# Kernel tuning notes

Hardware: AMD Instinct MI355X
Metric: run time of the kernel (lower is better)

Reference implementation:

```python
import jax, jax.numpy as jnp
import numpy as np

D_MODEL = 1024
NUM_HEADS = 16
HEAD_DIM = D_MODEL // NUM_HEADS
D_FF = 4096
LN_EPS = 1e-6  # flax nnx.LayerNorm default


def setup_inputs() -> dict:
    key = jax.random.key(0)
    ks = jax.random.split(key, 13)
    s_in = 1.0 / np.sqrt(D_MODEL)
    s_ff = 1.0 / np.sqrt(D_FF)
    return {
        "x": jax.random.normal(ks[0], (2, 2048, D_MODEL), dtype=jnp.float32),
        "Wq": jax.random.normal(ks[1], (D_MODEL, D_MODEL), jnp.float32) * s_in,
        "bq": jnp.zeros((D_MODEL,), jnp.float32),
        "Wk": jax.random.normal(ks[2], (D_MODEL, D_MODEL), jnp.float32) * s_in,
        "bk": jnp.zeros((D_MODEL,), jnp.float32),
        "Wv": jax.random.normal(ks[3], (D_MODEL, D_MODEL), jnp.float32) * s_in,
        "bv": jnp.zeros((D_MODEL,), jnp.float32),
        "Wo": jax.random.normal(ks[4], (D_MODEL, D_MODEL), jnp.float32) * s_in,
        "bo": jnp.zeros((D_MODEL,), jnp.float32),
        "W1": jax.random.normal(ks[5], (D_MODEL, D_FF), jnp.float32) * s_in,
        "b1": jnp.zeros((D_FF,), jnp.float32),
        "W2": jax.random.normal(ks[6], (D_FF, D_MODEL), jnp.float32) * s_ff,
        "b2": jnp.zeros((D_MODEL,), jnp.float32),
        "ln1_scale": jnp.ones((D_MODEL,), jnp.float32),
        "ln1_bias": jnp.zeros((D_MODEL,), jnp.float32),
        "ln2_scale": jnp.ones((D_MODEL,), jnp.float32),
        "ln2_bias": jnp.zeros((D_MODEL,), jnp.float32),
    }


def layer_norm(x, scale, bias):
    mu = jnp.mean(x, axis=-1, keepdims=True)
    var = jnp.mean(jnp.square(x - mu), axis=-1, keepdims=True)
    return (x - mu) * jax.lax.rsqrt(var + LN_EPS) * scale + bias


def reference(x, Wq, bq, Wk, bk, Wv, bv, Wo, bo, W1, b1, W2, b2,
              ln1_scale, ln1_bias, ln2_scale, ln2_bias):
    B, S, _ = x.shape
    h = layer_norm(x, ln1_scale, ln1_bias)
    # project and split heads: [B, H, S, Dh]
    q = (h @ Wq + bq).reshape(B, S, NUM_HEADS, HEAD_DIM).transpose(0, 2, 1, 3)
    k = (h @ Wk + bk).reshape(B, S, NUM_HEADS, HEAD_DIM).transpose(0, 2, 1, 3)
    v = (h @ Wv + bv).reshape(B, S, NUM_HEADS, HEAD_DIM).transpose(0, 2, 1, 3)
    scores = jnp.einsum("bhqd,bhkd->bhqk", q, k) / jnp.sqrt(jnp.float32(HEAD_DIM))
    attn = jax.nn.softmax(scores, axis=-1)
    out = jnp.einsum("bhqk,bhkd->bhqd", attn, v)
    out = out.transpose(0, 2, 1, 3).reshape(B, S, D_MODEL)
    x = x + out @ Wo + bo
    h2 = layer_norm(x, ln2_scale, ln2_bias)
    ff = jax.nn.relu(h2 @ W1 + b1) @ W2 + b2
    return x + ff
```

## Files before the change

kernel.cpp:

```cpp
#include <hip/hip_runtime.h>

typedef unsigned short ushort_t;
typedef __attribute__((ext_vector_type(8))) __bf16 bf16x8;
typedef __attribute__((ext_vector_type(8))) unsigned short ushort8v;
typedef __attribute__((ext_vector_type(4))) float floatx4;

__device__ inline float b2f(ushort_t u) {
    union { unsigned int i; float f; } c; c.i = ((unsigned int)u) << 16; return c.f;
}
__device__ inline ushort_t f2b(float f) {
    union { float f; unsigned int i; } c; c.f = f;
    unsigned int i = c.i;
    unsigned int r = (i + 0x7FFFu + ((i >> 16) & 1u)) >> 16;
    return (ushort_t)r;
}
__device__ inline bf16x8 as_bf16x8(ushort8v u) { return __builtin_bit_cast(bf16x8, u); }

__global__ __launch_bounds__(256) void concat3_kernel(
    const float* __restrict__ a, const float* __restrict__ b,
    const float* __restrict__ c, float* __restrict__ o) {
    int t = blockIdx.x * 256 + threadIdx.x;
    if (t < 3072)
        o[t] = t < 1024 ? a[t] : (t < 2048 ? b[t - 1024] : c[t - 2048]);
}

__global__ __launch_bounds__(256) void copy_f32_kernel(
    const float* __restrict__ src, float* __restrict__ dst) {
    size_t i = ((size_t)blockIdx.x * 256 + threadIdx.x) * 4;
    *(float4*)(dst + i) = *(const float4*)(src + i);
}

__global__ __launch_bounds__(256) void transpose_conv_kernel(
    const float* __restrict__ in, ushort_t* __restrict__ out,
    int R, int Csub, int ldin) {
    __shared__ float tile[32][33];
    int tx = threadIdx.x, ty = threadIdx.y;
    int r0 = blockIdx.y * 32, c0 = blockIdx.x * 32;
#pragma unroll
    for (int i = 0; i < 32; i += 8)
        tile[ty + i][tx] = in[(size_t)(r0 + ty + i) * ldin + c0 + tx];
    __syncthreads();
#pragma unroll
    for (int i = 0; i < 32; i += 8)
        out[(size_t)(c0 + ty + i) * R + r0 + tx] = f2b(tile[tx][ty + i]);
}

__global__ __launch_bounds__(256) void transpose_v_kernel(
    const ushort_t* __restrict__ qkv, ushort_t* __restrict__ vt) {
    __shared__ ushort_t tile[32][33];
    int tx = threadIdx.x, ty = threadIdx.y;
    int s0 = blockIdx.x * 32, d0 = blockIdx.y * 32;
    int bh = blockIdx.z, b = bh >> 4, h = bh & 15;
    const ushort_t* src = qkv + (size_t)b * 2048 * 3072 + 2048 + h * 64;
    ushort_t* dst = vt + (size_t)bh * 64 * 2048;
#pragma unroll
    for (int i = 0; i < 32; i += 8)
        tile[ty + i][tx] = src[(size_t)(s0 + ty + i) * 3072 + d0 + tx];
    __syncthreads();
#pragma unroll
    for (int i = 0; i < 32; i += 8)
        dst[(size_t)(d0 + ty + i) * 2048 + s0 + tx] = tile[tx][ty + i];
}

__device__ inline float wave_sum(float s) {
#pragma unroll
    for (int o = 32; o > 0; o >>= 1) s += __shfl_xor(s, o);
    return s;
}

__global__ __launch_bounds__(256) void ln_f32_kernel(
    const float* __restrict__ x, const float* __restrict__ sc,
    const float* __restrict__ bi, ushort_t* __restrict__ out) {
    int row = blockIdx.x, t = threadIdx.x;
    const float* xr = x + (size_t)row * 1024;
    float4 u = *(const float4*)(xr + t * 4);
    float v0 = u.x, v1 = u.y, v2 = u.z, v3 = u.w;
    __shared__ float sm[8];
    int wv = t >> 6, lane = t & 63;
    float s = wave_sum(v0 + v1 + v2 + v3);
    if (lane == 0) sm[wv] = s;
    __syncthreads();
    float mean = (sm[0] + sm[1] + sm[2] + sm[3]) * (1.0f / 1024.0f);
    float d0 = v0 - mean, d1 = v1 - mean, d2 = v2 - mean, d3 = v3 - mean;
    float q = wave_sum(d0 * d0 + d1 * d1 + d2 * d2 + d3 * d3);
    if (lane == 0) sm[4 + wv] = q;
    __syncthreads();
    float var = (sm[4] + sm[5] + sm[6] + sm[7]) * (1.0f / 1024.0f);
    float rn = rsqrtf(var + 1e-6f);
    float4 us = *(const float4*)(sc + t * 4);
    float4 ub = *(const float4*)(bi + t * 4);
    ushort4 o;
    o.x = f2b(d0 * rn * us.x + ub.x);
    o.y = f2b(d1 * rn * us.y + ub.y);
    o.z = f2b(d2 * rn * us.z + ub.z);
    o.w = f2b(d3 * rn * us.w + ub.w);
    *(ushort4*)(out + (size_t)row * 1024 + t * 4) = o;
}

__global__ __launch_bounds__(256) void gemm_bt_kernel(
    const ushort_t* __restrict__ A, const ushort_t* __restrict__ Bt,
    const float* __restrict__ bias, const float* __restrict__ resf,
    ushort_t* __restrict__ Cb, float* __restrict__ Cf,
    int M, int N, int K, int ldb, int op) {
    __shared__ __align__(16) ushort_t As[128 * 40];
    __shared__ __align__(16) ushort_t Bs[128 * 40];
    int tid = threadIdx.x;
    int m0 = blockIdx.y * 128, n0 = blockIdx.x * 128;
    int wv = tid >> 6, lane = tid & 63;
    int wr = wv & 1, wc = wv >> 1;
    int mo = wr * 64, no = wc * 64;
    int quad = lane >> 4, l16 = lane & 15;
    int k8 = quad * 8;

    floatx4 acc[4][4] = {};

    for (int k0 = 0; k0 < K; k0 += 32) {
#pragma unroll
        for (int c = 0; c < 2; ++c) {
            int e = c * 2048 + tid * 8;
            int r = e >> 5, kk = e & 31;
            *(ushort8v*)(As + r * 40 + kk) = *(const ushort8v*)(A + (size_t)(m0 + r) * K + k0 + kk);
            *(ushort8v*)(Bs + r * 40 + kk) = *(const ushort8v*)(Bt + (size_t)(n0 + r) * ldb + k0 + kk);
        }
        __syncthreads();
        bf16x8 af[4], bfr[4];
#pragma unroll
        for (int i = 0; i < 4; ++i) {
            af[i]  = as_bf16x8(*(const ushort8v*)(As + (mo + i * 16 + l16) * 40 + k8));
            bfr[i] = as_bf16x8(*(const ushort8v*)(Bs + (no + i * 16 + l16) * 40 + k8));
        }
#pragma unroll
        for (int mi = 0; mi < 4; ++mi)
#pragma unroll
            for (int ni = 0; ni < 4; ++ni)
                acc[mi][ni] = __builtin_amdgcn_mfma_f32_16x16x32_bf16(
                    af[mi], bfr[ni], acc[mi][ni], 0, 0, 0);
        __syncthreads();
    }

#pragma unroll
    for (int mi = 0; mi < 4; ++mi) {
#pragma unroll
        for (int r = 0; r < 4; ++r) {
            int row = m0 + mo + mi * 16 + quad * 4 + r;
            size_t rowoff = (size_t)row * N;
#pragma unroll
            for (int ni = 0; ni < 4; ++ni) {
                int col = n0 + no + ni * 16 + l16;
                float val = acc[mi][ni][r];
                if (op != 3) val += bias[col];
                if (op == 1) val = fmaxf(val, 0.0f);
                if (op >= 2) {
                    val += resf[rowoff + col];
                    Cf[rowoff + col] = val;
                } else {
                    Cb[rowoff + col] = f2b(val);
                }
            }
        }
    }
}

__global__ __launch_bounds__(256) void gemm_bt_atomic_kernel(
    const ushort_t* __restrict__ A, const ushort_t* __restrict__ Bt,
    const float* __restrict__ bias, float* __restrict__ Cf,
    int M, int N, int lda, int ldb, int Kc) {
    __shared__ __align__(16) ushort_t As[128 * 40];
    __shared__ __align__(16) ushort_t Bs[128 * 40];
    int tid = threadIdx.x;
    int m0 = blockIdx.y * 128, n0 = blockIdx.x * 128;
    int kbase = blockIdx.z * Kc;
    int wv = tid >> 6, lane = tid & 63;
    int wr = wv & 1, wc = wv >> 1;
    int mo = wr * 64, no = wc * 64;
    int quad = lane >> 4, l16 = lane & 15;
    int k8 = quad * 8;

    floatx4 acc[4][4] = {};

    for (int k0 = kbase; k0 < kbase + Kc; k0 += 32) {
#pragma unroll
        for (int c = 0; c < 2; ++c) {
            int e = c * 2048 + tid * 8;
            int r = e >> 5, kk = e & 31;
            *(ushort8v*)(As + r * 40 + kk) = *(const ushort8v*)(A + (size_t)(m0 + r) * lda + k0 + kk);
            *(ushort8v*)(Bs + r * 40 + kk) = *(const ushort8v*)(Bt + (size_t)(n0 + r) * ldb + k0 + kk);
        }
        __syncthreads();
        bf16x8 af[4], bfr[4];
#pragma unroll
        for (int i = 0; i < 4; ++i) {
            af[i]  = as_bf16x8(*(const ushort8v*)(As + (mo + i * 16 + l16) * 40 + k8));
            bfr[i] = as_bf16x8(*(const ushort8v*)(Bs + (no + i * 16 + l16) * 40 + k8));
        }
#pragma unroll
        for (int mi = 0; mi < 4; ++mi)
#pragma unroll
            for (int ni = 0; ni < 4; ++ni)
                acc[mi][ni] = __builtin_amdgcn_mfma_f32_16x16x32_bf16(
                    af[mi], bfr[ni], acc[mi][ni], 0, 0, 0);
        __syncthreads();
    }

    bool addb = (blockIdx.z == 0) && (bias != nullptr);
#pragma unroll
    for (int mi = 0; mi < 4; ++mi) {
#pragma unroll
        for (int r = 0; r < 4; ++r) {
            int row = m0 + mo + mi * 16 + quad * 4 + r;
            size_t rowoff = (size_t)row * N;
#pragma unroll
            for (int ni = 0; ni < 4; ++ni) {
                int col = n0 + no + ni * 16 + l16;
                float val = acc[mi][ni][r];
                if (addb) val += bias[col];
                unsafeAtomicAdd(&Cf[rowoff + col], val);
            }
        }
    }
}

__global__ __launch_bounds__(256) void attn_kernel(
    const ushort_t* __restrict__ qkv, const ushort_t* __restrict__ vt,
    ushort_t* __restrict__ om) {
    const int LDQ = 3072, LDO = 1024;
    int bh = blockIdx.y;
    int b = bh >> 4, h = bh & 15;
    size_t qbase = (size_t)b * 2048 * LDQ + h * 64;
    size_t kbase = qbase + 1024;
    const ushort_t* vtp = vt + (size_t)bh * 64 * 2048;
    int q0 = blockIdx.x * 128;
    int tid = threadIdx.x, wv = tid >> 6, lane = tid & 63;
    int quad = lane >> 4, l16 = lane & 15;
    int k8 = quad * 8;

    __shared__ __align__(16) ushort_t Ks[64 * 72];
    __shared__ __align__(16) ushort_t Vs[64 * 72];
    __shared__ __align__(16) ushort_t Ps[4 * 32 * 76];
    ushort_t* ps = Ps + wv * 32 * 76;

    int sr0 = tid >> 3, scc0 = (tid & 7) * 8;
    int sr1 = sr0 + 32;

    bf16x8 qf[2][2];
#pragma unroll
    for (int mt = 0; mt < 2; ++mt) {
        const ushort_t* qptr = qkv + qbase + (size_t)(q0 + wv * 32 + mt * 16 + l16) * LDQ;
        qf[mt][0] = as_bf16x8(*(const ushort8v*)(qptr + k8));
        qf[mt][1] = as_bf16x8(*(const ushort8v*)(qptr + 32 + k8));
    }

    bf16x8 ones;
#pragma unroll
    for (int j = 0; j < 8; ++j) ones[j] = (__bf16)1.0f;

    floatx4 Oacc[2][4] = {};
    floatx4 lsum[2] = {};

    ushort8v kreg0, kreg1, vreg0, vreg1;
    kreg0 = *(const ushort8v*)(qkv + kbase + (size_t)sr0 * LDQ + scc0);
    kreg1 = *(const ushort8v*)(qkv + kbase + (size_t)sr1 * LDQ + scc0);
    vreg0 = *(const ushort8v*)(vtp + (size_t)sr0 * 2048 + scc0);
    vreg1 = *(const ushort8v*)(vtp + (size_t)sr1 * 2048 + scc0);

    for (int kb = 0; kb < 2048; kb += 64) {
        __syncthreads();
        *(ushort8v*)(Ks + sr0 * 72 + scc0) = kreg0;
        *(ushort8v*)(Ks + sr1 * 72 + scc0) = kreg1;
        *(ushort8v*)(Vs + sr0 * 72 + scc0) = vreg0;
        *(ushort8v*)(Vs + sr1 * 72 + scc0) = vreg1;
        __syncthreads();

        int nkb = (kb + 64 < 2048) ? kb + 64 : 0;
        kreg0 = *(const ushort8v*)(qkv + kbase + (size_t)(nkb + sr0) * LDQ + scc0);
        kreg1 = *(const ushort8v*)(qkv + kbase + (size_t)(nkb + sr1) * LDQ + scc0);
        vreg0 = *(const ushort8v*)(vtp + (size_t)sr0 * 2048 + nkb + scc0);
        vreg1 = *(const ushort8v*)(vtp + (size_t)sr1 * 2048 + nkb + scc0);

        bf16x8 kf[4][2];
#pragma unroll
        for (int kt = 0; kt < 4; ++kt)
#pragma unroll
            for (int ds = 0; ds < 2; ++ds)
                kf[kt][ds] = as_bf16x8(
                    *(const ushort8v*)(Ks + (kt * 16 + l16) * 72 + ds * 32 + k8));

        floatx4 sc[2][4];
#pragma unroll
        for (int mt = 0; mt < 2; ++mt)
#pragma unroll
            for (int kt = 0; kt < 4; ++kt) {
                floatx4 s = {0.0f, 0.0f, 0.0f, 0.0f};
                s = __builtin_amdgcn_mfma_f32_16x16x32_bf16(qf[mt][0], kf[kt][0], s, 0, 0, 0);
                s = __builtin_amdgcn_mfma_f32_16x16x32_bf16(qf[mt][1], kf[kt][1], s, 0, 0, 0);
                sc[mt][kt] = s;
            }

#pragma unroll
        for (int mt = 0; mt < 2; ++mt)
#pragma unroll
            for (int kt = 0; kt < 4; ++kt)
#pragma unroll
                for (int r = 0; r < 4; ++r)
                    ps[(mt * 16 + quad * 4 + r) * 76 + kt * 16 + l16] =
                        f2b(__expf(sc[mt][kt][r] * 0.125f));

        bf16x8 vf[4][2];
#pragma unroll
        for (int dt = 0; dt < 4; ++dt)
#pragma unroll
            for (int ks = 0; ks < 2; ++ks)
                vf[dt][ks] = as_bf16x8(
                    *(const ushort8v*)(Vs + (dt * 16 + l16) * 72 + ks * 32 + k8));
#pragma unroll
        for (int mt = 0; mt < 2; ++mt) {
            bf16x8 pf0 = as_bf16x8(*(const ushort8v*)(ps + (mt * 16 + l16) * 76 + k8));
            bf16x8 pf1 = as_bf16x8(*(const ushort8v*)(ps + (mt * 16 + l16) * 76 + 32 + k8));
#pragma unroll
            for (int dt = 0; dt < 4; ++dt) {
                Oacc[mt][dt] = __builtin_amdgcn_mfma_f32_16x16x32_bf16(pf0, vf[dt][0], Oacc[mt][dt], 0, 0, 0);
                Oacc[mt][dt] = __builtin_amdgcn_mfma_f32_16x16x32_bf16(pf1, vf[dt][1], Oacc[mt][dt], 0, 0, 0);
            }
            lsum[mt] = __builtin_amdgcn_mfma_f32_16x16x32_bf16(pf0, ones, lsum[mt], 0, 0, 0);
            lsum[mt] = __builtin_amdgcn_mfma_f32_16x16x32_bf16(pf1, ones, lsum[mt], 0, 0, 0);
        }
    }

#pragma unroll
    for (int mt = 0; mt < 2; ++mt)
#pragma unroll
        for (int r = 0; r < 4; ++r) {
            float inv = 1.0f / lsum[mt][r];
            size_t rowoff = (size_t)(b * 2048 + q0 + wv * 32 + mt * 16 + quad * 4 + r) * LDO + h * 64;
#pragma unroll
            for (int dt = 0; dt < 4; ++dt)
                om[rowoff + dt * 16 + l16] = f2b(Oacc[mt][dt][r] * inv);
        }
}

extern "C" void kernel_launch(void* const* d_in, const int* in_sizes, int n_in,
                              void* d_out, int out_size, void* d_ws, size_t ws_size,
                              hipStream_t stream) {
    const float* x    = (const float*)d_in[0];
    const float* Wq   = (const float*)d_in[1];
    const float* bq   = (const float*)d_in[2];
    const float* Wk   = (const float*)d_in[3];
    const float* bk   = (const float*)d_in[4];
    const float* Wv   = (const float*)d_in[5];
    const float* bv   = (const float*)d_in[6];
    const float* Wo   = (const float*)d_in[7];
    const float* bo   = (const float*)d_in[8];
    const float* W1   = (const float*)d_in[9];
    const float* b1   = (const float*)d_in[10];
    const float* W2   = (const float*)d_in[11];
    const float* b2   = (const float*)d_in[12];
    const float* ln1s = (const float*)d_in[13];
    const float* ln1b = (const float*)d_in[14];
    const float* ln2s = (const float*)d_in[15];
    const float* ln2b = (const float*)d_in[16];
    float*    outf = (float*)d_out;
    ushort_t* ws   = (ushort_t*)d_ws;

    const size_t M1 = 1048576;
    ushort_t* qkvT    = ws;
    ushort_t* WoT     = ws + 3 * M1;
    ushort_t* W1T     = ws + 4 * M1;
    ushort_t* W2T     = ws + 8 * M1;
    ushort_t* h       = ws + 12 * M1;
    ushort_t* attnout = ws + 12 * M1;
    ushort_t* qkv     = ws + 16 * M1;
    ushort_t* h2      = ws;
    ushort_t* ffbuf   = ws + 12 * M1;
    float*    bqkv    = (float*)d_out;
    ushort_t* vtbuf   = (ushort_t*)d_out;

    dim3 tb(32, 8);
    dim3 tg(32, 32);

    concat3_kernel<<<12, 256, 0, stream>>>(bq, bk, bv, bqkv);
    transpose_conv_kernel<<<tg, tb, 0, stream>>>(Wq, qkvT,           1024, 1024, 1024);
    transpose_conv_kernel<<<tg, tb, 0, stream>>>(Wk, qkvT + 1 * M1,  1024, 1024, 1024);
    transpose_conv_kernel<<<tg, tb, 0, stream>>>(Wv, qkvT + 2 * M1,  1024, 1024, 1024);
    transpose_conv_kernel<<<tg, tb, 0, stream>>>(Wo, WoT,            1024, 1024, 1024);
    transpose_conv_kernel<<<dim3(128, 32), tb, 0, stream>>>(W1, W1T, 1024, 4096, 4096);
    transpose_conv_kernel<<<dim3(32, 128), tb, 0, stream>>>(W2, W2T, 4096, 1024, 1024);

    ln_f32_kernel<<<4096, 256, 0, stream>>>(x, ln1s, ln1b, h);

    gemm_bt_kernel<<<dim3(24, 32), 256, 0, stream>>>(
        h, qkvT, bqkv, nullptr, qkv, nullptr, 4096, 3072, 1024, 1024, 0);

    transpose_v_kernel<<<dim3(64, 2, 32), tb, 0, stream>>>(qkv, vtbuf);

    attn_kernel<<<dim3(16, 32), 256, 0, stream>>>(qkv, vtbuf, attnout);

    copy_f32_kernel<<<4096, 256, 0, stream>>>(x, outf);
    gemm_bt_atomic_kernel<<<dim3(8, 32, 4), 256, 0, stream>>>(
        attnout, WoT, bo, outf, 4096, 1024, 1024, 1024, 256);

    ln_f32_kernel<<<4096, 256, 0, stream>>>(outf, ln2s, ln2b, h2);

    gemm_bt_kernel<<<dim3(32, 32), 256, 0, stream>>>(
        h2, W1T, b1, nullptr, ffbuf, nullptr, 4096, 4096, 1024, 1024, 1);

    gemm_bt_atomic_kernel<<<dim3(8, 32, 4), 256, 0, stream>>>(
        ffbuf, W2T, b2, outf, 4096, 1024, 4096, 4096, 1024);
}
```

Baseline: 538.7 us.

## Use direct global-to-LDS loads with K=64 tiles and fuse weight transposes

GEMM kernels now stage A/B tiles via global_load_lds directly into unpadded LDS with a 64-wide K step, halving barriers per K. The six weight transpose launches are merged into one kernel, and the W2 split-K factor drops from 4 to 2 to reduce atomics. Unpadded LDS rows risk bank conflicts on fragment reads.

After: 520.8 us. -3.3%, faster.

```diff
diff --git a/kernel.cpp b/kernel.cpp
--- a/kernel.cpp
+++ b/kernel.cpp
@@ -15,6 +15,12 @@
     return (ushort_t)r;
 }
 __device__ inline bf16x8 as_bf16x8(ushort8v u) { return __builtin_bit_cast(bf16x8, u); }
+
+__device__ inline void load_lds16(const ushort_t* g, ushort_t* l) {
+    __builtin_amdgcn_global_load_lds(
+        (const __attribute__((address_space(1))) void*)g,
+        (__attribute__((address_space(3))) void*)l, 16, 0, 0);
+}
 
 __global__ __launch_bounds__(256) void concat3_kernel(
     const float* __restrict__ a, const float* __restrict__ b,
@@ -30,19 +36,39 @@
     *(float4*)(dst + i) = *(const float4*)(src + i);
 }
 
-__global__ __launch_bounds__(256) void transpose_conv_kernel(
-    const float* __restrict__ in, ushort_t* __restrict__ out,
-    int R, int Csub, int ldin) {
+__global__ __launch_bounds__(256) void transpose_all_kernel(
+    const float* __restrict__ Wq, const float* __restrict__ Wk,
+    const float* __restrict__ Wv, const float* __restrict__ Wo,
+    const float* __restrict__ W1, const float* __restrict__ W2,
+    ushort_t* __restrict__ dq, ushort_t* __restrict__ dk,
+    ushort_t* __restrict__ dv, ushort_t* __restrict__ do_,
+    ushort_t* __restrict__ d1, ushort_t* __restrict__ d2) {
+    int t = blockIdx.x;
+    const float* src; ushort_t* dst; int R, ld, tcx, tcy;
+    if (t < 4096) {
+        int id = t >> 10, u = t & 1023;
+        tcx = u & 31; tcy = u >> 5; R = 1024; ld = 1024;
+        src = id == 0 ? Wq : id == 1 ? Wk : id == 2 ? Wv : Wo;
+        dst = id == 0 ? dq : id == 1 ? dk : id == 2 ? dv : do_;
+    } else if (t < 8192) {
+        int u = t - 4096;
+        tcx = u & 127; tcy = u >> 7; R = 1024; ld = 4096;
+        src = W1; dst = d1;
+    } else {
+        int u = t - 8192;
+        tcx = u & 31; tcy = u >> 5; R = 4096; ld = 1024;
+        src = W2; dst = d2;
+    }
     __shared__ float tile[32][33];
     int tx = threadIdx.x, ty = threadIdx.y;
-    int r0 = blockIdx.y * 32, c0 = blockIdx.x * 32;
+    int r0 = tcy * 32, c0 = tcx * 32;
 #pragma unroll
     for (int i = 0; i < 32; i += 8)
-        tile[ty + i][tx] = in[(size_t)(r0 + ty + i) * ldin + c0 + tx];
+        tile[ty + i][tx] = src[(size_t)(r0 + ty + i) * ld + c0 + tx];
     __syncthreads();
 #pragma unroll
     for (int i = 0; i < 32; i += 8)
-        out[(size_t)(c0 + ty + i) * R + r0 + tx] = f2b(tile[tx][ty + i]);
+        dst[(size_t)(c0 + ty + i) * R + r0 + tx] = f2b(tile[tx][ty + i]);
 }
 
 __global__ __launch_bounds__(256) void transpose_v_kernel(
@@ -102,8 +128,8 @@
     const float* __restrict__ bias, const float* __restrict__ resf,
     ushort_t* __restrict__ Cb, float* __restrict__ Cf,
     int M, int N, int K, int ldb, int op) {
-    __shared__ __align__(16) ushort_t As[128 * 40];
-    __shared__ __align__(16) ushort_t Bs[128 * 40];
+    __shared__ __align__(16) ushort_t As[128 * 64];
+    __shared__ __align__(16) ushort_t Bs[128 * 64];
     int tid = threadIdx.x;
     int m0 = blockIdx.y * 128, n0 = blockIdx.x * 128;
     int wv = tid >> 6, lane = tid & 63;
@@ -114,27 +140,31 @@
 
     floatx4 acc[4][4] = {};
 
-    for (int k0 = 0; k0 < K; k0 += 32) {
-#pragma unroll
-        for (int c = 0; c < 2; ++c) {
+    for (int k0 = 0; k0 < K; k0 += 64) {
+#pragma unroll
+        for (int c = 0; c < 4; ++c) {
             int e = c * 2048 + tid * 8;
-            int r = e >> 5, kk = e & 31;
-            *(ushort8v*)(As + r * 40 + kk) = *(const ushort8v*)(A + (size_t)(m0 + r) * K + k0 + kk);
-            *(ushort8v*)(Bs + r * 40 + kk) = *(const ushort8v*)(Bt + (size_t)(n0 + r) * ldb + k0 + kk);
-        }
-        __syncthreads();
-        bf16x8 af[4], bfr[4];
-#pragma unroll
-        for (int i = 0; i < 4; ++i) {
-            af[i]  = as_bf16x8(*(const ushort8v*)(As + (mo + i * 16 + l16) * 40 + k8));
-            bfr[i] = as_bf16x8(*(const ushort8v*)(Bs + (no + i * 16 + l16) * 40 + k8));
-        }
-#pragma unroll
-        for (int mi = 0; mi < 4; ++mi)
-#pragma unroll
-            for (int ni = 0; ni < 4; ++ni)
-                acc[mi][ni] = __builtin_amdgcn_mfma_f32_16x16x32_bf16(
-                    af[mi], bfr[ni], acc[mi][ni], 0, 0, 0);
+            int r = e >> 6, kk = e & 63;
+            int wbase = c * 2048 + wv * 512;
+            load_lds16(A + (size_t)(m0 + r) * K + k0 + kk, As + wbase);
+            load_lds16(Bt + (size_t)(n0 + r) * ldb + k0 + kk, Bs + wbase);
+        }
+        __syncthreads();
+#pragma unroll
+        for (int h = 0; h < 2; ++h) {
+            bf16x8 af[4], bfr[4];
+#pragma unroll
+            for (int i = 0; i < 4; ++i) {
+                af[i]  = as_bf16x8(*(const ushort8v*)(As + (mo + i * 16 + l16) * 64 + h * 32 + k8));
+                bfr[i] = as_bf16x8(*(const ushort8v*)(Bs + (no + i * 16 + l16) * 64 + h * 32 + k8));
+            }
+#pragma unroll
+            for (int mi = 0; mi < 4; ++mi)
+#pragma unroll
+                for (int ni = 0; ni < 4; ++ni)
+                    acc[mi][ni] = __builtin_amdgcn_mfma_f32_16x16x32_bf16(
+                        af[mi], bfr[ni], acc[mi][ni], 0, 0, 0);
+        }
         __syncthreads();
     }
 
@@ -165,8 +195,8 @@
     const ushort_t* __restrict__ A, const ushort_t* __restrict__ Bt,
     const float* __restrict__ bias, float* __restrict__ Cf,
     int M, int N, int lda, int ldb, int Kc) {
-    __shared__ __align__(16) ushort_t As[128 * 40];
-    __shared__ __align__(16) ushort_t Bs[128 * 40];
+    __shared__ __align__(16) ushort_t As[128 * 64];
+    __shared__ __align__(16) ushort_t Bs[128 * 64];
     int tid = threadIdx.x;
     int m0 = blockIdx.y * 128, n0 = blockIdx.x * 128;
     int kbase = blockIdx.z * Kc;
@@ -178,27 +208,31 @@
 
     floatx4 acc[4][4] = {};
 
-    for (int k0 = kbase; k0 < kbase + Kc; k0 += 32) {
-#pragma unroll
-        for (int c = 0; c < 2; ++c) {
+    for (int k0 = kbase; k0 < kbase + Kc; k0 += 64) {
+#pragma unroll
+        for (int c = 0; c < 4; ++c) {
             int e = c * 2048 + tid * 8;
-            int r = e >> 5, kk = e & 31;
-            *(ushort8v*)(As + r * 40 + kk) = *(const ushort8v*)(A + (size_t)(m0 + r) * lda + k0 + kk);
-            *(ushort8v*)(Bs + r * 40 + kk) = *(const ushort8v*)(Bt + (size_t)(n0 + r) * ldb + k0 + kk);
-        }
-        __syncthreads();
-        bf16x8 af[4], bfr[4];
-#pragma unroll
-        for (int i = 0; i < 4; ++i) {
-            af[i]  = as_bf16x8(*(const ushort8v*)(As + (mo + i * 16 + l16) * 40 + k8));
-            bfr[i] = as_bf16x8(*(const ushort8v*)(Bs + (no + i * 16 + l16) * 40 + k8));
-        }
-#pragma unroll
-        for (int mi = 0; mi < 4; ++mi)
-#pragma unroll
-            for (int ni = 0; ni < 4; ++ni)
-                acc[mi][ni] = __builtin_amdgcn_mfma_f32_16x16x32_bf16(
-                    af[mi], bfr[ni], acc[mi][ni], 0, 0, 0);
+            int r = e >> 6, kk = e & 63;
+            int wbase = c * 2048 + wv * 512;
+            load_lds16(A + (size_t)(m0 + r) * lda + k0 + kk, As + wbase);
+            load_lds16(Bt + (size_t)(n0 + r) * ldb + k0 + kk, Bs + wbase);
+        }
+        __syncthreads();
+#pragma unroll
+        for (int h = 0; h < 2; ++h) {
+            bf16x8 af[4], bfr[4];
+#pragma unroll
+            for (int i = 0; i < 4; ++i) {
+                af[i]  = as_bf16x8(*(const ushort8v*)(As + (mo + i * 16 + l16) * 64 + h * 32 + k8));
+                bfr[i] = as_bf16x8(*(const ushort8v*)(Bs + (no + i * 16 + l16) * 64 + h * 32 + k8));
+            }
+#pragma unroll
+            for (int mi = 0; mi < 4; ++mi)
+#pragma unroll
+                for (int ni = 0; ni < 4; ++ni)
+                    acc[mi][ni] = __builtin_amdgcn_mfma_f32_16x16x32_bf16(
+                        af[mi], bfr[ni], acc[mi][ni], 0, 0, 0);
+        }
         __syncthreads();
     }
 
@@ -375,15 +409,11 @@
     ushort_t* vtbuf   = (ushort_t*)d_out;
 
     dim3 tb(32, 8);
-    dim3 tg(32, 32);
 
     concat3_kernel<<<12, 256, 0, stream>>>(bq, bk, bv, bqkv);
-    transpose_conv_kernel<<<tg, tb, 0, stream>>>(Wq, qkvT,           1024, 1024, 1024);
-    transpose_conv_kernel<<<tg, tb, 0, stream>>>(Wk, qkvT + 1 * M1,  1024, 1024, 1024);
-    transpose_conv_kernel<<<tg, tb, 0, stream>>>(Wv, qkvT + 2 * M1,  1024, 1024, 1024);
-    transpose_conv_kernel<<<tg, tb, 0, stream>>>(Wo, WoT,            1024, 1024, 1024);
-    transpose_conv_kernel<<<dim3(128, 32), tb, 0, stream>>>(W1, W1T, 1024, 4096, 4096);
-    transpose_conv_kernel<<<dim3(32, 128), tb, 0, stream>>>(W2, W2T, 4096, 1024, 1024);
+    transpose_all_kernel<<<12288, tb, 0, stream>>>(
+        Wq, Wk, Wv, Wo, W1, W2,
+        qkvT, qkvT + M1, qkvT + 2 * M1, WoT, W1T, W2T);
 
     ln_f32_kernel<<<4096, 256, 0, stream>>>(x, ln1s, ln1b, h);
 
@@ -403,6 +433,6 @@
     gemm_bt_kernel<<<dim3(32, 32), 256, 0, stream>>>(
         h2, W1T, b1, nullptr, ffbuf, nullptr, 4096, 4096, 1024, 1024, 1);
 
-    gemm_bt_atomic_kernel<<<dim3(8, 32, 4), 256, 0, stream>>>(
-        ffbuf, W2T, b2, outf, 4096, 1024, 4096, 4096, 1024);
-}
+    gemm_bt_atomic_kernel<<<dim3(8, 32, 2), 256, 0, stream>>>(
+        ffbuf, W2T, b2, outf, 4096, 1024, 4096, 4096, 2048);
+}
```
